# Kernel tuning notes

Hardware: AMD Instinct MI355X
Metric: run time of the kernel (lower is better)

## Reference

```python
import jax, jax.numpy as jnp
import numpy as np

HIDDEN = 512
ENC = 512

def setup_inputs() -> dict:
    key = jax.random.key(0)
    k1, k2, k3, k4, k5 = jax.random.split(key, 5)
    decoder_hidden = jax.random.normal(k1, (256, HIDDEN), dtype=jnp.float32)
    encoder_outputs = jax.random.normal(k2, (256, 1024, ENC), dtype=jnp.float32)
    s = 1.0 / np.sqrt(HIDDEN)
    W_h = jax.random.uniform(k3, (HIDDEN, HIDDEN), minval=-s, maxval=s, dtype=jnp.float32)
    W_s = jax.random.uniform(k4, (HIDDEN, ENC), minval=-s, maxval=s, dtype=jnp.float32)
    v = jax.random.uniform(k5, (1, HIDDEN), minval=-s, maxval=s, dtype=jnp.float32)
    return {"decoder_hidden": decoder_hidden, "encoder_outputs": encoder_outputs,
            "W_h": W_h, "W_s": W_s, "v": v}

def reference(decoder_hidden, encoder_outputs, W_h, W_s, v):
    # proj_h: (b, hidden); proj_s: (b, l, hidden)
    proj_h = decoder_hidden @ W_h.T
    proj_s = jnp.einsum('ble,he->blh', encoder_outputs, W_s)
    # additive score: v^T tanh(W_h h + W_s s_i) -> (b, l)
    scores = jnp.einsum('blh,h->bl', jnp.tanh(proj_h[:, None, :] + proj_s), v[0])
    alpha = jax.nn.softmax(scores, axis=-1)
    context = jnp.einsum('bl,ble->be', alpha, encoder_outputs)
    return (context, alpha)
```

## Files before the change

kernel.cpp:

```cpp
#include <hip/hip_runtime.h>
#include <hip/hip_bf16.h>

#define HID 512
#define ENCD 512
#define NB 256
#define SEQ 1024
#define M_TOTAL (NB * SEQ)

typedef short bf16x8 __attribute__((ext_vector_type(8)));
typedef float floatx4 __attribute__((ext_vector_type(4)));

__device__ __forceinline__ unsigned short f2bf(float f) {
    unsigned u = __builtin_bit_cast(unsigned, f);
    u += 0x7FFFu + ((u >> 16) & 1u);
    return (unsigned short)(u >> 16);
}

__device__ __forceinline__ bf16x8 pack8(float4 a, float4 b) {
    bf16x8 r;
    r[0] = (short)f2bf(a.x); r[1] = (short)f2bf(a.y);
    r[2] = (short)f2bf(a.z); r[3] = (short)f2bf(a.w);
    r[4] = (short)f2bf(b.x); r[5] = (short)f2bf(b.y);
    r[6] = (short)f2bf(b.z); r[7] = (short)f2bf(b.w);
    return r;
}

__global__ __launch_bounds__(256) void prep_kernel(
    const float* __restrict__ dh,
    const float* __restrict__ W_h,
    const float* __restrict__ W_s,
    float* __restrict__ proj_h,
    unsigned short* __restrict__ Ws_bf)
{
    __shared__ float sdh[2][HID];
    const int blk = blockIdx.x;
    const int t = threadIdx.x;
    const int b0 = blk * 2;

    {
        float4 d = ((const float4*)(dh + (size_t)b0 * HID))[t];
        ((float4*)&sdh[0][0])[t] = d;
    }

    #pragma unroll
    for (int i = 0; i < 2; ++i) {
        int f4 = (blk * 256 + t) * 2 + i;
        float4 w = ((const float4*)W_s)[f4];
        ushort4 o;
        o.x = f2bf(w.x); o.y = f2bf(w.y); o.z = f2bf(w.z); o.w = f2bf(w.w);
        ((ushort4*)Ws_bf)[f4] = o;
    }
    __syncthreads();

    #pragma unroll
    for (int i = 0; i < 2; ++i) {
        const int h = t + i * 256;
        const float4* wr = (const float4*)(W_h + (size_t)h * HID);
        float acc0 = 0.f, acc1 = 0.f;
        #pragma unroll 8
        for (int e4 = 0; e4 < HID / 4; ++e4) {
            float4 w  = wr[e4];
            float4 s0 = ((const float4*)&sdh[0][0])[e4];
            float4 s1 = ((const float4*)&sdh[1][0])[e4];
            acc0 += w.x * s0.x + w.y * s0.y + w.z * s0.z + w.w * s0.w;
            acc1 += w.x * s1.x + w.y * s1.y + w.z * s1.z + w.w * s1.w;
        }
        proj_h[(size_t)b0 * HID + h]       = acc0;
        proj_h[(size_t)(b0 + 1) * HID + h] = acc1;
    }
}

__global__ __launch_bounds__(512, 2) void score_gemm(
    const float* __restrict__ enc,
    const unsigned short* __restrict__ Ws,
    const float* __restrict__ proj_h,
    const float* __restrict__ v,
    float* __restrict__ scores)
{
    __shared__ float sred[4][128];

    const int t    = threadIdx.x;
    const int wave = t >> 6;
    const int lane = t & 63;
    const int ln15 = lane & 15;
    const int lk   = lane >> 4;
    const int m0   = blockIdx.x * 128;
    const int bb   = m0 >> 10;
    const int wm   = (wave & 1) * 64;
    const int wn   = (wave >> 1) * 128;

    floatx4 acc[4][8] = {};

    const float* ap[4];
    #pragma unroll
    for (int mi = 0; mi < 4; ++mi)
        ap[mi] = enc + (size_t)(m0 + wm + mi * 16 + ln15) * ENCD + lk * 8;

    const unsigned short* bp = Ws + (size_t)(wn + ln15) * HID + lk * 8;

    float4 a0[4], a1[4];
    #pragma unroll
    for (int mi = 0; mi < 4; ++mi) {
        a0[mi] = *(const float4*)(ap[mi]);
        a1[mi] = *(const float4*)(ap[mi] + 4);
    }

    #pragma unroll 2
    for (int kt = 0; kt < 16; ++kt) {
        const int k0 = kt * 32;

        bf16x8 bfrag[8];
        #pragma unroll
        for (int nj = 0; nj < 8; ++nj)
            bfrag[nj] = *(const bf16x8*)(bp + (size_t)nj * 16 * HID + k0);

        bf16x8 afrag[4];
        #pragma unroll
        for (int mi = 0; mi < 4; ++mi)
            afrag[mi] = pack8(a0[mi], a1[mi]);

        if (kt < 15) {
            #pragma unroll
            for (int mi = 0; mi < 4; ++mi) {
                a0[mi] = *(const float4*)(ap[mi] + k0 + 32);
                a1[mi] = *(const float4*)(ap[mi] + k0 + 36);
            }
        }

        #pragma unroll
        for (int mi = 0; mi < 4; ++mi)
            #pragma unroll
            for (int nj = 0; nj < 8; ++nj)
                acc[mi][nj] = __builtin_amdgcn_mfma_f32_16x16x32_bf16(
                    afrag[mi], bfrag[nj], acc[mi][nj], 0, 0, 0);
    }

    float phv[8], vv[8];
    #pragma unroll
    for (int nj = 0; nj < 8; ++nj) {
        const int n = wn + nj * 16 + ln15;
        phv[nj] = proj_h[bb * HID + n];
        vv[nj]  = v[n];
    }

    #pragma unroll
    for (int mi = 0; mi < 4; ++mi) {
        #pragma unroll
        for (int r = 0; r < 4; ++r) {
            float s = 0.f;
            #pragma unroll
            for (int nj = 0; nj < 8; ++nj) {
                float x = acc[mi][nj][r] + phv[nj];
                float e = __expf(2.f * x);
                float th = 1.f - 2.f / (e + 1.f);
                s += vv[nj] * th;
            }
            s += __shfl_xor(s, 8, 64);
            s += __shfl_xor(s, 4, 64);
            s += __shfl_xor(s, 2, 64);
            s += __shfl_xor(s, 1, 64);
            if (ln15 == 0) {
                const int row = wm + mi * 16 + lk * 4 + r;
                sred[wave >> 1][row] = s;
            }
        }
    }
    __syncthreads();
    if (t < 128)
        scores[m0 + t] = sred[0][t] + sred[1][t] + sred[2][t] + sred[3][t];
}

__global__ __launch_bounds__(1024) void softmax_ctx(
    const float* __restrict__ scores,
    const float* __restrict__ enc,
    float* __restrict__ ctx_out,
    float* __restrict__ alpha_out)
{
    __shared__ float salpha[SEQ];
    __shared__ float sctx[8][ENCD];
    __shared__ float sbufA[16], sbufB[16];
    const int b = blockIdx.x;
    const int t = threadIdx.x;
    const int w = t >> 6;

    float sc = scores[(size_t)b * SEQ + t];

    float mx = sc;
    #pragma unroll
    for (int m = 32; m >= 1; m >>= 1) mx = fmaxf(mx, __shfl_xor(mx, m, 64));
    if ((t & 63) == 0) sbufA[w] = mx;
    __syncthreads();
    float gm = sbufA[0];
    #pragma unroll
    for (int i = 1; i < 16; ++i) gm = fmaxf(gm, sbufA[i]);

    float e0 = __expf(sc - gm);
    float ssum = e0;
    #pragma unroll
    for (int m = 32; m >= 1; m >>= 1) ssum += __shfl_xor(ssum, m, 64);
    if ((t & 63) == 0) sbufB[w] = ssum;
    __syncthreads();
    float tot = 0.f;
    #pragma unroll
    for (int i = 0; i < 16; ++i) tot += sbufB[i];
    const float inv = 1.f / tot;

    const float a0 = e0 * inv;
    salpha[t] = a0;
    alpha_out[(size_t)b * SEQ + t] = a0;
    __syncthreads();

    const int tx = t & 127;
    const int ty = t >> 7;
    float4 acc = make_float4(0.f, 0.f, 0.f, 0.f);
    const float* ep = enc + (size_t)b * SEQ * ENCD + (size_t)tx * 4;
    #pragma unroll 8
    for (int l = ty; l < SEQ; l += 8) {
        float4 vv = *(const float4*)(ep + (size_t)l * ENCD);
        float a = salpha[l];
        acc.x += a * vv.x; acc.y += a * vv.y;
        acc.z += a * vv.z; acc.w += a * vv.w;
    }
    *(float4*)(&sctx[ty][tx * 4]) = acc;
    __syncthreads();

    if (t < ENCD) {
        float s = 0.f;
        #pragma unroll
        for (int y = 0; y < 8; ++y) s += sctx[y][t];
        ctx_out[(size_t)b * ENCD + t] = s;
    }
}

extern "C" void kernel_launch(void* const* d_in, const int* in_sizes, int n_in,
                              void* d_out, int out_size, void* d_ws, size_t ws_size,
                              hipStream_t stream) {
    const float* dh  = (const float*)d_in[0];
    const float* enc = (const float*)d_in[1];
    const float* W_h = (const float*)d_in[2];
    const float* W_s = (const float*)d_in[3];
    const float* v   = (const float*)d_in[4];

    float* ws = (float*)d_ws;
    float* proj_h = ws;
    float* scores = ws + 131072;
    unsigned short* Ws_bf = (unsigned short*)(ws + 131072 + 262144);

    float* ctx   = (float*)d_out;
    float* alpha = (float*)d_out + NB * HID;

    prep_kernel<<<128, 256, 0, stream>>>(dh, W_h, W_s, proj_h, Ws_bf);
    score_gemm<<<M_TOTAL / 128, 512, 0, stream>>>(enc, Ws_bf, proj_h, v, scores);
    softmax_ctx<<<NB, 1024, 0, stream>>>(scores, enc, ctx, alpha);
}
```

Baseline: 1.241 ms.

## Stage A tiles through LDS, pre-shuffle B fragments, split context across two blocks

The score GEMM now loads encoder rows with coalesced row-major reads, converts them to bf16 once into a padded, double-buffered LDS tile, and reads MFMA A fragments from LDS instead of strided per-lane global loads. W_s is pre-shuffled in the prep kernel into fragment order, so each lane's B load is contiguous. The softmax/context kernel launches two blocks per batch row, each covering half of the encoder dimension, to increase parallelism. The cost is a barrier per k-step, extra LDS use that may lower occupancy, and a softmax that is computed twice per row.

```diff
diff --git a/kernel.cpp b/kernel.cpp
--- a/kernel.cpp
+++ b/kernel.cpp
@@ -15,14 +15,8 @@
     u += 0x7FFFu + ((u >> 16) & 1u);
     return (unsigned short)(u >> 16);
 }
-
-__device__ __forceinline__ bf16x8 pack8(float4 a, float4 b) {
-    bf16x8 r;
-    r[0] = (short)f2bf(a.x); r[1] = (short)f2bf(a.y);
-    r[2] = (short)f2bf(a.z); r[3] = (short)f2bf(a.w);
-    r[4] = (short)f2bf(b.x); r[5] = (short)f2bf(b.y);
-    r[6] = (short)f2bf(b.z); r[7] = (short)f2bf(b.w);
-    return r;
+__device__ __forceinline__ ushort4 cvt4(float4 a) {
+    return make_ushort4(f2bf(a.x), f2bf(a.y), f2bf(a.z), f2bf(a.w));
 }
 
 __global__ __launch_bounds__(256) void prep_kernel(
@@ -30,25 +24,28 @@
     const float* __restrict__ W_h,
     const float* __restrict__ W_s,
     float* __restrict__ proj_h,
-    unsigned short* __restrict__ Ws_bf)
+    unsigned short* __restrict__ Bshuf)
 {
     __shared__ float sdh[2][HID];
     const int blk = blockIdx.x;
     const int t = threadIdx.x;
     const int b0 = blk * 2;
 
+    ((float4*)&sdh[0][0])[t] = ((const float4*)(dh + (size_t)b0 * HID))[t];
+
     {
-        float4 d = ((const float4*)(dh + (size_t)b0 * HID))[t];
-        ((float4*)&sdh[0][0])[t] = d;
-    }
-
-    #pragma unroll
-    for (int i = 0; i < 2; ++i) {
-        int f4 = (blk * 256 + t) * 2 + i;
-        float4 w = ((const float4*)W_s)[f4];
-        ushort4 o;
-        o.x = f2bf(w.x); o.y = f2bf(w.y); o.z = f2bf(w.z); o.w = f2bf(w.w);
-        ((ushort4*)Ws_bf)[f4] = o;
+        const int id   = blk * 256 + t;
+        const int lane = id & 63;
+        const int nj   = (id >> 6) & 7;
+        const int kt   = (id >> 9) & 15;
+        const int wnG  = id >> 13;
+        const int n = wnG * 128 + nj * 16 + (lane & 15);
+        const int k = kt * 32 + (lane >> 4) * 8;
+        const float* src = W_s + (size_t)n * HID + k;
+        float4 s0 = *(const float4*)src;
+        float4 s1 = *(const float4*)(src + 4);
+        *(ushort4*)(Bshuf + (size_t)id * 8)     = cvt4(s0);
+        *(ushort4*)(Bshuf + (size_t)id * 8 + 4) = cvt4(s1);
     }
     __syncthreads();
 
@@ -72,11 +69,12 @@
 
 __global__ __launch_bounds__(512, 2) void score_gemm(
     const float* __restrict__ enc,
-    const unsigned short* __restrict__ Ws,
+    const unsigned short* __restrict__ Bshuf,
     const float* __restrict__ proj_h,
     const float* __restrict__ v,
     float* __restrict__ scores)
 {
+    __shared__ unsigned short sA[2][128 * 40];
     __shared__ float sred[4][128];
 
     const int t    = threadIdx.x;
@@ -87,45 +85,46 @@
     const int m0   = blockIdx.x * 128;
     const int bb   = m0 >> 10;
     const int wm   = (wave & 1) * 64;
-    const int wn   = (wave >> 1) * 128;
+    const int wnG  = wave >> 1;
+    const int wn   = wnG * 128;
 
     floatx4 acc[4][8] = {};
 
-    const float* ap[4];
-    #pragma unroll
-    for (int mi = 0; mi < 4; ++mi)
-        ap[mi] = enc + (size_t)(m0 + wm + mi * 16 + ln15) * ENCD + lk * 8;
-
-    const unsigned short* bp = Ws + (size_t)(wn + ln15) * HID + lk * 8;
-
-    float4 a0[4], a1[4];
-    #pragma unroll
-    for (int mi = 0; mi < 4; ++mi) {
-        a0[mi] = *(const float4*)(ap[mi]);
-        a1[mi] = *(const float4*)(ap[mi] + 4);
-    }
-
-    #pragma unroll 2
+    const int r0 = t >> 3, c4 = t & 7;
+    const float* gA0 = enc + (size_t)(m0 + r0) * ENCD + c4 * 4;
+    const float* gA1 = gA0 + (size_t)64 * ENCD;
+    unsigned short* wp0 = &sA[0][r0 * 40 + c4 * 4];
+    unsigned short* wp1 = &sA[0][(r0 + 64) * 40 + c4 * 4];
+    const int bufStride = 128 * 40;
+
+    const unsigned short* bbase = Bshuf + ((size_t)wnG * 8192 + lane) * 8;
+
+    {
+        float4 p0 = *(const float4*)gA0;
+        float4 p1 = *(const float4*)gA1;
+        *(ushort4*)wp0 = cvt4(p0);
+        *(ushort4*)wp1 = cvt4(p1);
+    }
+    __syncthreads();
+
     for (int kt = 0; kt < 16; ++kt) {
-        const int k0 = kt * 32;
+        const int cur = kt & 1;
+
+        float4 n0, n1;
+        if (kt < 15) {
+            n0 = *(const float4*)(gA0 + (kt + 1) * 32);
+            n1 = *(const float4*)(gA1 + (kt + 1) * 32);
+        }
 
         bf16x8 bfrag[8];
         #pragma unroll
         for (int nj = 0; nj < 8; ++nj)
-            bfrag[nj] = *(const bf16x8*)(bp + (size_t)nj * 16 * HID + k0);
+            bfrag[nj] = *(const bf16x8*)(bbase + ((size_t)(kt * 8 + nj)) * 512);
 
         bf16x8 afrag[4];
         #pragma unroll
         for (int mi = 0; mi < 4; ++mi)
-            afrag[mi] = pack8(a0[mi], a1[mi]);
-
-        if (kt < 15) {
-            #pragma unroll
-            for (int mi = 0; mi < 4; ++mi) {
-                a0[mi] = *(const float4*)(ap[mi] + k0 + 32);
-                a1[mi] = *(const float4*)(ap[mi] + k0 + 36);
-            }
-        }
+            afrag[mi] = *(const bf16x8*)(&sA[cur][(wm + mi * 16 + ln15) * 40 + lk * 8]);
 
         #pragma unroll
         for (int mi = 0; mi < 4; ++mi)
@@ -133,6 +132,13 @@
             for (int nj = 0; nj < 8; ++nj)
                 acc[mi][nj] = __builtin_amdgcn_mfma_f32_16x16x32_bf16(
                     afrag[mi], bfrag[nj], acc[mi][nj], 0, 0, 0);
+
+        if (kt < 15) {
+            const int nb = 1 - cur;
+            *(ushort4*)(wp0 + nb * bufStride) = cvt4(n0);
+            *(ushort4*)(wp1 + nb * bufStride) = cvt4(n1);
+        }
+        __syncthreads();
     }
 
     float phv[8], vv[8];
@@ -159,10 +165,8 @@
             s += __shfl_xor(s, 4, 64);
             s += __shfl_xor(s, 2, 64);
             s += __shfl_xor(s, 1, 64);
-            if (ln15 == 0) {
-                const int row = wm + mi * 16 + lk * 4 + r;
-                sred[wave >> 1][row] = s;
-            }
+            if (ln15 == 0)
+                sred[wnG][wm + mi * 16 + lk * 4 + r] = s;
         }
     }
     __syncthreads();
@@ -177,9 +181,10 @@
     float* __restrict__ alpha_out)
 {
     __shared__ float salpha[SEQ];
-    __shared__ float sctx[8][ENCD];
+    __shared__ float sctx[16][256];
     __shared__ float sbufA[16], sbufB[16];
-    const int b = blockIdx.x;
+    const int b    = blockIdx.x >> 1;
+    const int half = blockIdx.x & 1;
     const int t = threadIdx.x;
     const int w = t >> 6;
 
@@ -207,15 +212,15 @@
 
     const float a0 = e0 * inv;
     salpha[t] = a0;
-    alpha_out[(size_t)b * SEQ + t] = a0;
-    __syncthreads();
-
-    const int tx = t & 127;
-    const int ty = t >> 7;
+    if (half == 0) alpha_out[(size_t)b * SEQ + t] = a0;
+    __syncthreads();
+
+    const int tx = t & 63;
+    const int ty = t >> 6;
     float4 acc = make_float4(0.f, 0.f, 0.f, 0.f);
-    const float* ep = enc + (size_t)b * SEQ * ENCD + (size_t)tx * 4;
+    const float* ep = enc + (size_t)b * SEQ * ENCD + half * 256 + (size_t)tx * 4;
     #pragma unroll 8
-    for (int l = ty; l < SEQ; l += 8) {
+    for (int l = ty; l < SEQ; l += 16) {
         float4 vv = *(const float4*)(ep + (size_t)l * ENCD);
         float a = salpha[l];
         acc.x += a * vv.x; acc.y += a * vv.y;
@@ -224,11 +229,11 @@
     *(float4*)(&sctx[ty][tx * 4]) = acc;
     __syncthreads();
 
-    if (t < ENCD) {
+    if (t < 256) {
         float s = 0.f;
         #pragma unroll
-        for (int y = 0; y < 8; ++y) s += sctx[y][t];
-        ctx_out[(size_t)b * ENCD + t] = s;
+        for (int y = 0; y < 16; ++y) s += sctx[y][t];
+        ctx_out[(size_t)b * ENCD + half * 256 + t] = s;
     }
 }
 
@@ -244,12 +249,12 @@
     float* ws = (float*)d_ws;
     float* proj_h = ws;
     float* scores = ws + 131072;
-    unsigned short* Ws_bf = (unsigned short*)(ws + 131072 + 262144);
+    unsigned short* Bshuf = (unsigned short*)(ws + 131072 + 262144);
 
     float* ctx   = (float*)d_out;
     float* alpha = (float*)d_out + NB * HID;
 
-    prep_kernel<<<128, 256, 0, stream>>>(dh, W_h, W_s, proj_h, Ws_bf);
-    score_gemm<<<M_TOTAL / 128, 512, 0, stream>>>(enc, Ws_bf, proj_h, v, scores);
-    softmax_ctx<<<NB, 1024, 0, stream>>>(scores, enc, ctx, alpha);
-}
+    prep_kernel<<<128, 256, 0, stream>>>(dh, W_h, W_s, proj_h, Bshuf);
+    score_gemm<<<M_TOTAL / 128, 512, 0, stream>>>(enc, Bshuf, proj_h, v, scores);
+    softmax_ctx<<<NB * 2, 1024, 0, stream>>>(scores, enc, ctx, alpha);
+}
```

Result: faster. 1.014 ms (-18.3%).
